# Optimization experiments

Hardware: AMD Instinct MI355X
Metric: run time of the kernel (lower is better)

The kernel has to match this reference:

```python
import jax, jax.numpy as jnp
import numpy as np

N_HEADS = 16


def setup_inputs() -> dict:
    key = jax.random.key(0)
    ks = jax.random.split(key, 8)
    ts, td, b, hc = 64, 4096, 8, 1024
    scale = 1.0 / np.sqrt(hc)
    return {
        "s": jax.random.normal(ks[0], (ts, b, hc), dtype=jnp.float32),
        "d": jax.random.normal(ks[1], (td, b, hc), dtype=jnp.float32),
        "Wq": jax.random.normal(ks[2], (hc, hc), dtype=jnp.float32) * scale,
        "bq": jax.random.normal(ks[3], (hc,), dtype=jnp.float32) * 0.01,
        "Wk": jax.random.normal(ks[4], (hc, hc), dtype=jnp.float32) * scale,
        "bk": jax.random.normal(ks[5], (hc,), dtype=jnp.float32) * 0.01,
        "Wv": jax.random.normal(ks[6], (hc, hc), dtype=jnp.float32) * scale,
        "bv": jax.random.normal(ks[7], (hc,), dtype=jnp.float32) * 0.01,
    }


def reference(s, d, Wq, bq, Wk, bk, Wv, bv):
    ts, b, hc = s.shape
    td = d.shape[0]
    h = N_HEADS
    c = hc // h
    # linear projections (torch Linear: x @ W.T + b)
    q = (s @ Wq.T + bq).reshape(ts, b, h, c)
    k = (d @ Wk.T + bk).reshape(td, b, h, c)
    v = (d @ Wv.T + bv).reshape(td, b, h, c)
    # scores over (slot, token) pairs, scaled
    a = jnp.einsum('sbhc,dbhc->sdbh', q, k) / jnp.sqrt(jnp.asarray(c, s.dtype))
    # competitive softmax across the SLOT axis (dim 0), not the key axis
    a = jax.nn.softmax(a, axis=0)          # (ts, td, b, h)
    n = jnp.sum(a, axis=1) + 0.001         # (ts, b, h)
    num = jnp.einsum('sdbh,dbhc->sbhc', a, v)
    out = num / n[..., None]               # normalized weighted average
    return out.reshape(ts, b, hc)
```

## Files before the change

### kernel.cpp

```cpp
#include <hip/hip_runtime.h>


#define TS 64
#define TD 4096
#define BATCH 8
#define HC 1024
#define NHEAD 16
#define MD (TD*BATCH)
#define MS (TS*BATCH)
#define NCHUNK 8
#define CHTOK (TD/NCHUNK)

#define KTILES 32

typedef __attribute__((ext_vector_type(8))) __bf16 bf16x8;
typedef __attribute__((ext_vector_type(4))) float f32x4;
typedef __attribute__((ext_vector_type(4))) unsigned short u16x4;
typedef __attribute__((ext_vector_type(8))) unsigned short u16x8;

__device__ __forceinline__ unsigned short f2bf(float x){
  union { float f; unsigned u; } v; v.f = x;
  unsigned r = v.u + 0x7FFFu + ((v.u >> 16) & 1u);
  return (unsigned short)(r >> 16);
}

__device__ __forceinline__ void gll16(const void* g, void* l){
  __builtin_amdgcn_global_load_lds((__attribute__((address_space(1))) void*)g,
                                   (__attribute__((address_space(3))) void*)l, 16, 0, 0);
}

__global__ void cvt_all(const float* __restrict__ d, const float* __restrict__ s,
                        const float* __restrict__ wq, const float* __restrict__ wk,
                        const float* __restrict__ wv,
                        unsigned short* __restrict__ dbf, unsigned short* __restrict__ sbf,
                        unsigned short* __restrict__ wqb, unsigned short* __restrict__ wkb,
                        unsigned short* __restrict__ wvb){
  long i = (long)blockIdx.x * 256 + threadIdx.x;
  const float* src; unsigned short* dst; long off;
  if (i < 8388608L)      { src = d;  dst = dbf; off = i; }
  else if (i < 8519680L) { src = s;  dst = sbf; off = i - 8388608L; }
  else if (i < 8781824L) { src = wq; dst = wqb; off = i - 8519680L; }
  else if (i < 9043968L) { src = wk; dst = wkb; off = i - 8781824L; }
  else                   { src = wv; dst = wvb; off = i - 9043968L; }
  f32x4 f = ((const f32x4*)src)[off];
  u16x4 o;
  o[0] = f2bf(f[0]); o[1] = f2bf(f[1]); o[2] = f2bf(f[2]); o[3] = f2bf(f[3]);
  ((u16x4*)dst)[off] = o;
}

__global__ __launch_bounds__(512, 2) void gemm_qkv(
    const unsigned short* __restrict__ A,
    const unsigned short* __restrict__ Sb,
    const unsigned short* __restrict__ Wkv,
    const unsigned short* __restrict__ Wq,
    const float* __restrict__ bq,
    const float* __restrict__ bk,
    const float* __restrict__ bv,
    unsigned short* __restrict__ Qout,
    unsigned short* __restrict__ Kout,
    unsigned short* __restrict__ Vout)
{
  __shared__ unsigned short As[4][256*32];
  __shared__ unsigned short Bs[4][256*32];

  const int nwg = gridDim.x;
  const int cpx = nwg >> 3;
  const int orig = blockIdx.x;
  const int wg = (orig & 7) * cpx + (orig >> 3);
  const int tid = threadIdx.x;
  const int lane = tid & 63, w = tid >> 6;
  const int l15 = lane & 15, lg = lane >> 4;
  const int wm = w >> 2, wn = w & 3;

  const bool isQ = (wg >= 1024);
  int mt, nt;
  const unsigned short* Ab; const unsigned short* Bb;
  if (!isQ){ mt = wg >> 3; nt = wg & 7; Ab = A;  Bb = Wkv; }
  else     { int qi = wg - 1024; mt = qi >> 2; nt = qi & 3; Ab = Sb; Bb = Wq; }

  const int lr = lane >> 2;
  const int schunk = (((lane & 3) ^ ((lane >> 3) & 3)) << 4);
  const char* pa[2]; const char* pb[2]; unsigned ldso[2];
  #pragma unroll
  for (int j = 0; j < 2; ++j){
    int grow = j*128 + w*16 + lr;
    pa[j] = (const char*)Ab + (size_t)(mt*256 + grow)*2048 + schunk;
    pb[j] = (const char*)Bb + (size_t)(nt*256 + grow)*2048 + schunk;
    ldso[j] = (unsigned)(j*8192 + w*1024);
  }

  #define STAGE_A(t) { char* dst = (char*)&As[(t)&3][0]; \
    gll16(pa[0] + (size_t)(t)*64, dst + ldso[0]); \
    gll16(pa[1] + (size_t)(t)*64, dst + ldso[1]); }
  #define STAGE_B(t) { char* dst = (char*)&Bs[(t)&3][0]; \
    gll16(pb[0] + (size_t)(t)*64, dst + ldso[0]); \
    gll16(pb[1] + (size_t)(t)*64, dst + ldso[1]); }

  const unsigned cswz = ((unsigned)(lg ^ ((l15 >> 1) & 3))) << 4;
  const unsigned aoff = (unsigned)(wm*128 + l15)*64 + cswz;
  const unsigned boff = (unsigned)(wn*64  + l15)*64 + cswz;

  const f32x4 fz = {0.f, 0.f, 0.f, 0.f};
  f32x4 acc[8][4];
  #pragma unroll
  for (int m = 0; m < 8; ++m)
    #pragma unroll
    for (int n = 0; n < 4; ++n) acc[m][n] = fz;

  STAGE_A(0) STAGE_B(0) STAGE_A(1) STAGE_B(1) STAGE_A(2) STAGE_B(2)
  asm volatile("s_waitcnt vmcnt(8)" ::: "memory");
  __builtin_amdgcn_s_barrier();
  __builtin_amdgcn_sched_barrier(0);

  #pragma unroll 1
  for (int t = 0; t < KTILES; ++t){
    const char* as = (const char*)&As[t & 3][0];
    const char* bs = (const char*)&Bs[t & 3][0];

    bf16x8 af0[4], bfr[4];
    #pragma unroll
    for (int mf = 0; mf < 4; ++mf) af0[mf] = *(const bf16x8*)(as + aoff + mf*1024u);
    #pragma unroll
    for (int nf = 0; nf < 4; ++nf) bfr[nf] = *(const bf16x8*)(bs + boff + nf*1024u);
    if (t + 3 < KTILES) STAGE_A(t + 3)
    __builtin_amdgcn_s_setprio(1);
    #pragma unroll
    for (int mf = 0; mf < 4; ++mf)
      #pragma unroll
      for (int nf = 0; nf < 4; ++nf)
        acc[mf][nf] = __builtin_amdgcn_mfma_f32_16x16x32_bf16(af0[mf], bfr[nf], acc[mf][nf], 0, 0, 0);
    __builtin_amdgcn_s_setprio(0);

    bf16x8 af1[4];
    #pragma unroll
    for (int mf = 0; mf < 4; ++mf) af1[mf] = *(const bf16x8*)(as + aoff + (4 + mf)*1024u);
    if (t + 3 < KTILES) STAGE_B(t + 3)
    __builtin_amdgcn_s_setprio(1);
    #pragma unroll
    for (int mf = 0; mf < 4; ++mf)
      #pragma unroll
      for (int nf = 0; nf < 4; ++nf)
        acc[4 + mf][nf] = __builtin_amdgcn_mfma_f32_16x16x32_bf16(af1[mf], bfr[nf], acc[4 + mf][nf], 0, 0, 0);
    __builtin_amdgcn_s_setprio(0);

    __builtin_amdgcn_sched_barrier(0);
    if (t < KTILES - 3)       { asm volatile("s_waitcnt vmcnt(8)" ::: "memory"); }
    else if (t == KTILES - 3) { asm volatile("s_waitcnt vmcnt(4)" ::: "memory"); }
    else if (t == KTILES - 2) { asm volatile("s_waitcnt vmcnt(0)" ::: "memory"); }
    __builtin_amdgcn_s_barrier();
    __builtin_amdgcn_sched_barrier(0);
  }

  int ccol; unsigned short* Cb; const float* bias;
  if (isQ)         { Cb = Qout; bias = bq; ccol = nt*256 + wn*64; }
  else if (nt < 4) { Cb = Kout; bias = bk; ccol = (nt & 3)*256 + wn*64; }
  else             { Cb = Vout; bias = bv; ccol = (nt & 3)*256 + wn*64; }
  float bvv[4];
  #pragma unroll
  for (int nf = 0; nf < 4; ++nf) bvv[nf] = bias[ccol + nf*16 + l15];
  #pragma unroll
  for (int mf = 0; mf < 8; ++mf){
    #pragma unroll
    for (int r = 0; r < 4; ++r){
      size_t row = (size_t)(mt*256 + wm*128 + mf*16 + lg*4 + r);
      unsigned short* cp = Cb + row*1024 + ccol;
      #pragma unroll
      for (int nf = 0; nf < 4; ++nf)
        cp[nf*16 + l15] = f2bf(acc[mf][nf][r] + bvv[nf]);
    }
  }
  #undef STAGE_A
  #undef STAGE_B
}

__global__ __launch_bounds__(256) void attn_kernel(
    const unsigned short* __restrict__ Q,
    const unsigned short* __restrict__ K,
    const unsigned short* __restrict__ V,
    float* __restrict__ P)
{
  __shared__ unsigned short Qs[64*64];
  __shared__ unsigned short Ks[64*64];
  __shared__ unsigned short Vt[80*64];
  __shared__ unsigned short Al[64*64];
  __shared__ float red[256];

  const int bh = blockIdx.x;
  const int chunk = blockIdx.y;
  const int bb = bh >> 4, h = bh & 15;
  const int tid = threadIdx.x;
  const int lane = tid & 63, w = tid >> 6;
  const int l15 = lane & 15, lg = lane >> 4;
  const int lrow = lane >> 3, lch = (lane & 7) << 4;

  for (int i = tid; i < 16*64; i += 256){
    int r = i >> 6;
    Vt[(64 + r)*64 + (i & 63)] = (r == 0) ? (unsigned short)0x3F80 : (unsigned short)0;
  }

  #pragma unroll
  for (int j = 0; j < 2; ++j){
    int row = w*16 + j*8 + lrow;
    int sw = lch ^ ((row & 7) << 4);
    const char* g = (const char*)Q + (size_t)(row*BATCH + bb)*2048 + h*128 + sw;
    gll16(g, (char*)Qs + (w*16 + j*8)*128);
  }

  const f32x4 fz = {0.f, 0.f, 0.f, 0.f};
  f32x4 acc[5];
  #pragma unroll
  for (int nb = 0; nb < 5; ++nb) acc[nb] = fz;

  const int vtok = tid >> 2;
  const int vcg  = tid & 3;
  const int t0 = chunk * CHTOK;

  for (int tt = 0; tt < CHTOK/64; ++tt){
    const int tb = t0 + tt*64;
    #pragma unroll
    for (int j = 0; j < 2; ++j){
      int row = w*16 + j*8 + lrow;
      int sw = lch ^ ((row & 7) << 4);
      const char* g = (const char*)K + (size_t)((size_t)(tb + row)*BATCH + bb)*2048 + h*128 + sw;
      gll16(g, (char*)Ks + (w*16 + j*8)*128);
    }
    const char* vg = (const char*)V + (size_t)((size_t)(tb + vtok)*BATCH + bb)*2048 + h*128 + vcg*32;
    u16x8 v0 = *(const u16x8*)vg;
    u16x8 v1 = *(const u16x8*)(vg + 16);
    __syncthreads();

    bf16x8 qa[2];
    #pragma unroll
    for (int kk = 0; kk < 2; ++kk){
      int row = w*16 + l15;
      qa[kk] = *(const bf16x8*)((const char*)Qs + row*128 + ((lg*16 + kk*64) ^ ((row & 7) << 4)));
    }
    float e[4][4];
    #pragma unroll
    for (int nb = 0; nb < 4; ++nb){
      f32x4 s = fz;
      #pragma unroll
      for (int kk = 0; kk < 2; ++kk){
        int row = nb*16 + l15;
        bf16x8 kb = *(const bf16x8*)((const char*)Ks + row*128 + ((lg*16 + kk*64) ^ ((row & 7) << 4)));
        s = __builtin_amdgcn_mfma_f32_16x16x32_bf16(qa[kk], kb, s, 0, 0, 0);
      }
      #pragma unroll
      for (int r = 0; r < 4; ++r) e[nb][r] = __expf(s[r] * 0.125f);
    }
    #pragma unroll
    for (int nb = 0; nb < 4; ++nb){
      float cp = e[nb][0] + e[nb][1] + e[nb][2] + e[nb][3];
      cp += __shfl_xor(cp, 16);
      cp += __shfl_xor(cp, 32);
      if (lg == 0) red[w*64 + nb*16 + l15] = cp;
    }
    __syncthreads();

    #pragma unroll
    for (int nb = 0; nb < 4; ++nb){
      int col = nb*16 + l15;
      float dn = red[col] + red[64 + col] + red[128 + col] + red[192 + col];
      float inv = 1.0f / dn;
      #pragma unroll
      for (int r = 0; r < 4; ++r){
        int row = w*16 + lg*4 + r;
        Al[row*64 + ((((2*col)) ^ ((row & 7) << 4)) >> 1)] = f2bf(e[nb][r] * inv);
      }
    }
    #pragma unroll
    for (int ee = 0; ee < 8; ++ee){
      int c0 = vcg*16 + ee;
      int sw0 = (((c0 & 7) ^ (c0 >> 3)) & 7) << 4;
      Vt[c0*64 + (((2*vtok) ^ sw0) >> 1)] = v0[ee];
    }
    #pragma unroll
    for (int ee = 0; ee < 8; ++ee){
      int c1 = vcg*16 + 8 + ee;
      int sw1 = (((c1 & 7) ^ (c1 >> 3)) & 7) << 4;
      Vt[c1*64 + (((2*vtok) ^ sw1) >> 1)] = v1[ee];
    }
    __syncthreads();

    bf16x8 aa[2];
    #pragma unroll
    for (int kk = 0; kk < 2; ++kk){
      int row = w*16 + l15;
      aa[kk] = *(const bf16x8*)((const char*)Al + row*128 + ((lg*16 + kk*64) ^ ((row & 7) << 4)));
    }
    #pragma unroll
    for (int nb = 0; nb < 5; ++nb){
      #pragma unroll
      for (int kk = 0; kk < 2; ++kk){
        int row = nb*16 + l15;
        int sw = (((row & 7) ^ (row >> 3)) & 7) << 4;
        bf16x8 vb = *(const bf16x8*)((const char*)Vt + row*128 + ((lg*16 + kk*64) ^ sw));
        acc[nb] = __builtin_amdgcn_mfma_f32_16x16x32_bf16(aa[kk], vb, acc[nb], 0, 0, 0);
      }
    }
  }

  float* Pb = P + (size_t)(bh*NCHUNK + chunk) * 64 * 80;
  #pragma unroll
  for (int nb = 0; nb < 5; ++nb){
    #pragma unroll
    for (int r = 0; r < 4; ++r){
      int s = w*16 + lg*4 + r;
      Pb[(size_t)s*80 + nb*16 + l15] = acc[nb][r];
    }
  }
}

__global__ void reduce_out(const float* __restrict__ P, float* __restrict__ out){
  int flat = blockIdx.x * 256 + threadIdx.x;
  int c = flat & 63, s = (flat >> 6) & 63, bh = flat >> 12;
  int bb = bh >> 4, h = bh & 15;
  float sc = 0.f, sn = 0.f;
  #pragma unroll
  for (int ch = 0; ch < NCHUNK; ++ch){
    const float* base = P + ((size_t)(bh*NCHUNK + ch)*64 + s)*80;
    sc += base[c];
    sn += base[64];
  }
  out[((size_t)s*BATCH + bb)*1024 + h*64 + c] = sc / (sn + 0.001f);
}

extern "C" void kernel_launch(void* const* d_in, const int* in_sizes, int n_in,
                              void* d_out, int out_size, void* d_ws, size_t ws_size,
                              hipStream_t stream)
{
  const float* s  = (const float*)d_in[0];
  const float* d  = (const float*)d_in[1];
  const float* Wq = (const float*)d_in[2];
  const float* bq = (const float*)d_in[3];
  const float* Wk = (const float*)d_in[4];
  const float* bk = (const float*)d_in[5];
  const float* Wv = (const float*)d_in[6];
  const float* bv = (const float*)d_in[7];
  float* out = (float*)d_out;

  char* ws = (char*)d_ws;
  unsigned short* dbf = (unsigned short*)(ws);
  unsigned short* sbf = (unsigned short*)(ws + 67108864);
  unsigned short* wqb = (unsigned short*)(ws + 68157440);
  unsigned short* wkb = (unsigned short*)(ws + 70254592);
  unsigned short* wvb = (unsigned short*)(ws + 72351744);
  unsigned short* Qw  = (unsigned short*)(ws + 74448896);
  unsigned short* Kw  = (unsigned short*)(ws + 75497472);
  unsigned short* Vw  = (unsigned short*)(ws + 142606336);
  float*          Pw  = (float*)(ws + 209715200);

  (void)in_sizes; (void)n_in; (void)out_size; (void)ws_size;

  cvt_all<<<36352, 256, 0, stream>>>(d, s, Wq, Wk, Wv, dbf, sbf, wqb, wkb, wvb);

  gemm_qkv<<<1032, 512, 0, stream>>>(dbf, sbf, wkb, wqb, bq, bk, bv, Qw, Kw, Vw);

  attn_kernel<<<dim3(128, NCHUNK), 256, 0, stream>>>(Qw, Kw, Vw, Pw);

  reduce_out<<<(TS*BATCH*HC)/256, 256, 0, stream>>>(Pw, out);
}
```

Before: 243.8 us.

## Fuse fp32-to-bf16 conversion of activations into QKV GEMM A-tile loading

Removes the separate conversion pass over d and s (about 128 MB read and 64 MB written). The GEMM now loads fp32 A tiles into registers one tile ahead, converts them to bf16 and writes them to LDS with the same swizzle. Only the weights still go through a small conversion kernel. In exchange, the GEMM reads twice as many A bytes, and since each d tile is read by 8 N-tile workgroups, that extra fp32 traffic depends on cache reuse. A prefetch depth shrinks from 3 stages to 1 with register staging, and each iteration adds an LDS write plus a wait.

```diff
diff --git a/kernel.cpp b/kernel.cpp
--- a/kernel.cpp
+++ b/kernel.cpp
@@ -29,19 +29,15 @@
                                    (__attribute__((address_space(3))) void*)l, 16, 0, 0);
 }
 
-__global__ void cvt_all(const float* __restrict__ d, const float* __restrict__ s,
-                        const float* __restrict__ wq, const float* __restrict__ wk,
-                        const float* __restrict__ wv,
-                        unsigned short* __restrict__ dbf, unsigned short* __restrict__ sbf,
-                        unsigned short* __restrict__ wqb, unsigned short* __restrict__ wkb,
-                        unsigned short* __restrict__ wvb){
+__global__ void cvt_w(const float* __restrict__ wq, const float* __restrict__ wk,
+                      const float* __restrict__ wv,
+                      unsigned short* __restrict__ wqb, unsigned short* __restrict__ wkb,
+                      unsigned short* __restrict__ wvb){
   long i = (long)blockIdx.x * 256 + threadIdx.x;
   const float* src; unsigned short* dst; long off;
-  if (i < 8388608L)      { src = d;  dst = dbf; off = i; }
-  else if (i < 8519680L) { src = s;  dst = sbf; off = i - 8388608L; }
-  else if (i < 8781824L) { src = wq; dst = wqb; off = i - 8519680L; }
-  else if (i < 9043968L) { src = wk; dst = wkb; off = i - 8781824L; }
-  else                   { src = wv; dst = wvb; off = i - 9043968L; }
+  if (i < 262144L)      { src = wq; dst = wqb; off = i; }
+  else if (i < 524288L) { src = wk; dst = wkb; off = i - 262144L; }
+  else                  { src = wv; dst = wvb; off = i - 524288L; }
   f32x4 f = ((const f32x4*)src)[off];
   u16x4 o;
   o[0] = f2bf(f[0]); o[1] = f2bf(f[1]); o[2] = f2bf(f[2]); o[3] = f2bf(f[3]);
@@ -49,8 +45,8 @@
 }
 
 __global__ __launch_bounds__(512, 2) void gemm_qkv(
-    const unsigned short* __restrict__ A,
-    const unsigned short* __restrict__ Sb,
+    const float* __restrict__ dA,
+    const float* __restrict__ sA,
     const unsigned short* __restrict__ Wkv,
     const unsigned short* __restrict__ Wq,
     const float* __restrict__ bq,
@@ -74,28 +70,52 @@
 
   const bool isQ = (wg >= 1024);
   int mt, nt;
-  const unsigned short* Ab; const unsigned short* Bb;
-  if (!isQ){ mt = wg >> 3; nt = wg & 7; Ab = A;  Bb = Wkv; }
-  else     { int qi = wg - 1024; mt = qi >> 2; nt = qi & 3; Ab = Sb; Bb = Wq; }
+  const float* Af; const unsigned short* Bb;
+  if (!isQ){ mt = wg >> 3; nt = wg & 7; Af = dA; Bb = Wkv; }
+  else     { int qi = wg - 1024; mt = qi >> 2; nt = qi & 3; Af = sA; Bb = Wq; }
+
+  const int lrw = lane >> 2;
+  const int c4  = lane & 3;
+  const int swp = c4 ^ ((lane >> 3) & 3);
+  const char* paf[2]; unsigned wadr[2];
+  #pragma unroll
+  for (int j = 0; j < 2; ++j){
+    int rowg = j*128 + w*16 + lrw;
+    paf[j] = (const char*)Af + (size_t)(mt*256 + rowg) * 4096 + (unsigned)(c4*32);
+    wadr[j] = (unsigned)(rowg*64 + (swp << 4));
+  }
 
   const int lr = lane >> 2;
   const int schunk = (((lane & 3) ^ ((lane >> 3) & 3)) << 4);
-  const char* pa[2]; const char* pb[2]; unsigned ldso[2];
+  const char* pb[2]; unsigned ldso[2];
   #pragma unroll
   for (int j = 0; j < 2; ++j){
     int grow = j*128 + w*16 + lr;
-    pa[j] = (const char*)Ab + (size_t)(mt*256 + grow)*2048 + schunk;
     pb[j] = (const char*)Bb + (size_t)(nt*256 + grow)*2048 + schunk;
     ldso[j] = (unsigned)(j*8192 + w*1024);
   }
 
-  #define STAGE_A(t) { char* dst = (char*)&As[(t)&3][0]; \
-    gll16(pa[0] + (size_t)(t)*64, dst + ldso[0]); \
-    gll16(pa[1] + (size_t)(t)*64, dst + ldso[1]); }
   #define STAGE_B(t) { char* dst = (char*)&Bs[(t)&3][0]; \
     gll16(pb[0] + (size_t)(t)*64, dst + ldso[0]); \
     gll16(pb[1] + (size_t)(t)*64, dst + ldso[1]); }
 
+  f32x4 la0, la1, la2, la3;
+  #define LOAD_A(tn) { \
+    la0 = *(const f32x4*)(paf[0] + (size_t)(tn)*128); \
+    la1 = *(const f32x4*)(paf[0] + (size_t)(tn)*128 + 16); \
+    la2 = *(const f32x4*)(paf[1] + (size_t)(tn)*128); \
+    la3 = *(const f32x4*)(paf[1] + (size_t)(tn)*128 + 16); }
+
+  #define CVT_WRITE_A(buf_) { \
+    char* dstA = (char*)&As[buf_][0]; \
+    bf16x8 t0, t1; \
+    t0[0]=(__bf16)la0[0]; t0[1]=(__bf16)la0[1]; t0[2]=(__bf16)la0[2]; t0[3]=(__bf16)la0[3]; \
+    t0[4]=(__bf16)la1[0]; t0[5]=(__bf16)la1[1]; t0[6]=(__bf16)la1[2]; t0[7]=(__bf16)la1[3]; \
+    t1[0]=(__bf16)la2[0]; t1[1]=(__bf16)la2[1]; t1[2]=(__bf16)la2[2]; t1[3]=(__bf16)la2[3]; \
+    t1[4]=(__bf16)la3[0]; t1[5]=(__bf16)la3[1]; t1[6]=(__bf16)la3[2]; t1[7]=(__bf16)la3[3]; \
+    *(bf16x8*)(dstA + wadr[0]) = t0; \
+    *(bf16x8*)(dstA + wadr[1]) = t1; }
+
   const unsigned cswz = ((unsigned)(lg ^ ((l15 >> 1) & 3))) << 4;
   const unsigned aoff = (unsigned)(wm*128 + l15)*64 + cswz;
   const unsigned boff = (unsigned)(wn*64  + l15)*64 + cswz;
@@ -107,8 +127,11 @@
     #pragma unroll
     for (int n = 0; n < 4; ++n) acc[m][n] = fz;
 
-  STAGE_A(0) STAGE_B(0) STAGE_A(1) STAGE_B(1) STAGE_A(2) STAGE_B(2)
-  asm volatile("s_waitcnt vmcnt(8)" ::: "memory");
+  STAGE_B(0) STAGE_B(1) STAGE_B(2)
+  LOAD_A(0)
+  CVT_WRITE_A(0)
+  asm volatile("s_waitcnt lgkmcnt(0)" ::: "memory");
+  __builtin_amdgcn_sched_barrier(0);
   __builtin_amdgcn_s_barrier();
   __builtin_amdgcn_sched_barrier(0);
 
@@ -117,12 +140,15 @@
     const char* as = (const char*)&As[t & 3][0];
     const char* bs = (const char*)&Bs[t & 3][0];
 
+    if (t + 1 < KTILES) { LOAD_A(t + 1) }
+    __builtin_amdgcn_sched_barrier(0);
+
     bf16x8 af0[4], bfr[4];
     #pragma unroll
     for (int mf = 0; mf < 4; ++mf) af0[mf] = *(const bf16x8*)(as + aoff + mf*1024u);
     #pragma unroll
     for (int nf = 0; nf < 4; ++nf) bfr[nf] = *(const bf16x8*)(bs + boff + nf*1024u);
-    if (t + 3 < KTILES) STAGE_A(t + 3)
+    if (t + 3 < KTILES) STAGE_B(t + 3)
     __builtin_amdgcn_s_setprio(1);
     #pragma unroll
     for (int mf = 0; mf < 4; ++mf)
@@ -134,7 +160,6 @@
     bf16x8 af1[4];
     #pragma unroll
     for (int mf = 0; mf < 4; ++mf) af1[mf] = *(const bf16x8*)(as + aoff + (4 + mf)*1024u);
-    if (t + 3 < KTILES) STAGE_B(t + 3)
     __builtin_amdgcn_s_setprio(1);
     #pragma unroll
     for (int mf = 0; mf < 4; ++mf)
@@ -144,8 +169,12 @@
     __builtin_amdgcn_s_setprio(0);
 
     __builtin_amdgcn_sched_barrier(0);
-    if (t < KTILES - 3)       { asm volatile("s_waitcnt vmcnt(8)" ::: "memory"); }
-    else if (t == KTILES - 3) { asm volatile("s_waitcnt vmcnt(4)" ::: "memory"); }
+    if (t + 1 < KTILES) { CVT_WRITE_A((t + 1) & 3) }
+    __builtin_amdgcn_sched_barrier(0);
+    asm volatile("s_waitcnt lgkmcnt(0)" ::: "memory");
+    __builtin_amdgcn_sched_barrier(0);
+    if (t < KTILES - 3)       { asm volatile("s_waitcnt vmcnt(4)" ::: "memory"); }
+    else if (t == KTILES - 3) { asm volatile("s_waitcnt vmcnt(2)" ::: "memory"); }
     else if (t == KTILES - 2) { asm volatile("s_waitcnt vmcnt(0)" ::: "memory"); }
     __builtin_amdgcn_s_barrier();
     __builtin_amdgcn_sched_barrier(0);
@@ -169,8 +198,9 @@
         cp[nf*16 + l15] = f2bf(acc[mf][nf][r] + bvv[nf]);
     }
   }
-  #undef STAGE_A
   #undef STAGE_B
+  #undef LOAD_A
+  #undef CVT_WRITE_A
 }
 
 __global__ __launch_bounds__(256) void attn_kernel(
@@ -340,8 +370,6 @@
   float* out = (float*)d_out;
 
   char* ws = (char*)d_ws;
-  unsigned short* dbf = (unsigned short*)(ws);
-  unsigned short* sbf = (unsigned short*)(ws + 67108864);
   unsigned short* wqb = (unsigned short*)(ws + 68157440);
   unsigned short* wkb = (unsigned short*)(ws + 70254592);
   unsigned short* wvb = (unsigned short*)(ws + 72351744);
@@ -352,9 +380,9 @@
 
   (void)in_sizes; (void)n_in; (void)out_size; (void)ws_size;
 
-  cvt_all<<<36352, 256, 0, stream>>>(d, s, Wq, Wk, Wv, dbf, sbf, wqb, wkb, wvb);
-
-  gemm_qkv<<<1032, 512, 0, stream>>>(dbf, sbf, wkb, wqb, bq, bk, bv, Qw, Kw, Vw);
+  cvt_w<<<3072, 256, 0, stream>>>(Wq, Wk, Wv, wqb, wkb, wvb);
+
+  gemm_qkv<<<1032, 512, 0, stream>>>(d, s, wkb, wqb, bq, bk, bv, Qw, Kw, Vw);
 
   attn_kernel<<<dim3(128, NCHUNK), 256, 0, stream>>>(Qw, Kw, Vw, Pw);
 
```

After: 304.8 us. 25.0% more time.

## Switch QKV GEMM to 64-wide K tiles with double buffering

Applied to the files above, without the earlier changes.

The QKV projection GEMM now stages K tiles of 64 instead of 32, with a 2-slot double buffer replacing the 4-slot ring (32KB per operand either way). The LDS swizzle is widened to 8 chunks, and the manual vmcnt waits and split A/B staging are replaced by a single combined stage and __syncthreads per iteration. This halves the number of barriers and loop iterations. In exchange the prefetch depth drops from three tiles ahead to one, and the __syncthreads waits on all outstanding loads, so global latency may be exposed.

```diff
diff --git a/kernel.cpp b/kernel.cpp
--- a/kernel.cpp
+++ b/kernel.cpp
@@ -11,7 +11,7 @@
 #define NCHUNK 8
 #define CHTOK (TD/NCHUNK)
 
-#define KTILES 32
+#define KT64 16
 
 typedef __attribute__((ext_vector_type(8))) __bf16 bf16x8;
 typedef __attribute__((ext_vector_type(4))) float f32x4;
@@ -60,8 +60,8 @@
     unsigned short* __restrict__ Kout,
     unsigned short* __restrict__ Vout)
 {
-  __shared__ unsigned short As[4][256*32];
-  __shared__ unsigned short Bs[4][256*32];
+  __shared__ unsigned short As[2][256*64];
+  __shared__ unsigned short Bs[2][256*64];
 
   const int nwg = gridDim.x;
   const int cpx = nwg >> 3;
@@ -78,27 +78,36 @@
   if (!isQ){ mt = wg >> 3; nt = wg & 7; Ab = A;  Bb = Wkv; }
   else     { int qi = wg - 1024; mt = qi >> 2; nt = qi & 3; Ab = Sb; Bb = Wq; }
 
-  const int lr = lane >> 2;
-  const int schunk = (((lane & 3) ^ ((lane >> 3) & 3)) << 4);
-  const char* pa[2]; const char* pb[2]; unsigned ldso[2];
-  #pragma unroll
-  for (int j = 0; j < 2; ++j){
-    int grow = j*128 + w*16 + lr;
+  const int ri = lane >> 3;
+  const int Sst = ((ri >> 1) & 3) | ((ri & 1) << 2);
+  const unsigned schunk = (unsigned)(((lane & 7) ^ Sst) << 4);
+  const char* pa[4]; const char* pb[4]; unsigned ldso[4];
+  #pragma unroll
+  for (int j = 0; j < 4; ++j){
+    int grow = w*32 + j*8 + ri;
     pa[j] = (const char*)Ab + (size_t)(mt*256 + grow)*2048 + schunk;
     pb[j] = (const char*)Bb + (size_t)(nt*256 + grow)*2048 + schunk;
-    ldso[j] = (unsigned)(j*8192 + w*1024);
-  }
-
-  #define STAGE_A(t) { char* dst = (char*)&As[(t)&3][0]; \
-    gll16(pa[0] + (size_t)(t)*64, dst + ldso[0]); \
-    gll16(pa[1] + (size_t)(t)*64, dst + ldso[1]); }
-  #define STAGE_B(t) { char* dst = (char*)&Bs[(t)&3][0]; \
-    gll16(pb[0] + (size_t)(t)*64, dst + ldso[0]); \
-    gll16(pb[1] + (size_t)(t)*64, dst + ldso[1]); }
-
-  const unsigned cswz = ((unsigned)(lg ^ ((l15 >> 1) & 3))) << 4;
-  const unsigned aoff = (unsigned)(wm*128 + l15)*64 + cswz;
-  const unsigned boff = (unsigned)(wn*64  + l15)*64 + cswz;
+    ldso[j] = (unsigned)((w*32 + j*8) * 128);
+  }
+
+  #define STAGE_AB(t_, sl_) { \
+    const size_t ko = (size_t)(t_) * 128; \
+    char* da = (char*)&As[sl_][0]; char* db = (char*)&Bs[sl_][0]; \
+    gll16(pa[0] + ko, da + ldso[0]); \
+    gll16(pa[1] + ko, da + ldso[1]); \
+    gll16(pa[2] + ko, da + ldso[2]); \
+    gll16(pa[3] + ko, da + ldso[3]); \
+    gll16(pb[0] + ko, db + ldso[0]); \
+    gll16(pb[1] + ko, db + ldso[1]); \
+    gll16(pb[2] + ko, db + ldso[2]); \
+    gll16(pb[3] + ko, db + ldso[3]); \
+    __builtin_amdgcn_sched_barrier(0); }
+
+  const int Sr = ((l15 >> 1) & 3) | ((l15 & 1) << 2);
+  const unsigned ck0 = (unsigned)(((0 + lg) ^ Sr) << 4);
+  const unsigned ck1 = (unsigned)(((4 + lg) ^ Sr) << 4);
+  const unsigned arow = (unsigned)(wm*128 + l15) * 128;
+  const unsigned brow = (unsigned)(wn*64  + l15) * 128;
 
   const f32x4 fz = {0.f, 0.f, 0.f, 0.f};
   f32x4 acc[8][4];
@@ -107,48 +116,41 @@
     #pragma unroll
     for (int n = 0; n < 4; ++n) acc[m][n] = fz;
 
-  STAGE_A(0) STAGE_B(0) STAGE_A(1) STAGE_B(1) STAGE_A(2) STAGE_B(2)
-  asm volatile("s_waitcnt vmcnt(8)" ::: "memory");
-  __builtin_amdgcn_s_barrier();
-  __builtin_amdgcn_sched_barrier(0);
+  #define HALF(as_, bs_, ckh_) { \
+    bf16x8 af0[4], bfr[4]; \
+    _Pragma("unroll") \
+    for (int mf = 0; mf < 4; ++mf) af0[mf] = *(const bf16x8*)(as_ + arow + mf*2048u + (ckh_)); \
+    _Pragma("unroll") \
+    for (int nf = 0; nf < 4; ++nf) bfr[nf] = *(const bf16x8*)(bs_ + brow + nf*2048u + (ckh_)); \
+    __builtin_amdgcn_s_setprio(1); \
+    _Pragma("unroll") \
+    for (int mf = 0; mf < 4; ++mf) \
+      _Pragma("unroll") \
+      for (int nf = 0; nf < 4; ++nf) \
+        acc[mf][nf] = __builtin_amdgcn_mfma_f32_16x16x32_bf16(af0[mf], bfr[nf], acc[mf][nf], 0, 0, 0); \
+    __builtin_amdgcn_s_setprio(0); \
+    bf16x8 af1[4]; \
+    _Pragma("unroll") \
+    for (int mf = 0; mf < 4; ++mf) af1[mf] = *(const bf16x8*)(as_ + arow + (4 + mf)*2048u + (ckh_)); \
+    __builtin_amdgcn_s_setprio(1); \
+    _Pragma("unroll") \
+    for (int mf = 0; mf < 4; ++mf) \
+      _Pragma("unroll") \
+      for (int nf = 0; nf < 4; ++nf) \
+        acc[4 + mf][nf] = __builtin_amdgcn_mfma_f32_16x16x32_bf16(af1[mf], bfr[nf], acc[4 + mf][nf], 0, 0, 0); \
+    __builtin_amdgcn_s_setprio(0); }
+
+  STAGE_AB(0, 0)
+  __syncthreads();
 
   #pragma unroll 1
-  for (int t = 0; t < KTILES; ++t){
-    const char* as = (const char*)&As[t & 3][0];
-    const char* bs = (const char*)&Bs[t & 3][0];
-
-    bf16x8 af0[4], bfr[4];
-    #pragma unroll
-    for (int mf = 0; mf < 4; ++mf) af0[mf] = *(const bf16x8*)(as + aoff + mf*1024u);
-    #pragma unroll
-    for (int nf = 0; nf < 4; ++nf) bfr[nf] = *(const bf16x8*)(bs + boff + nf*1024u);
-    if (t + 3 < KTILES) STAGE_A(t + 3)
-    __builtin_amdgcn_s_setprio(1);
-    #pragma unroll
-    for (int mf = 0; mf < 4; ++mf)
-      #pragma unroll
-      for (int nf = 0; nf < 4; ++nf)
-        acc[mf][nf] = __builtin_amdgcn_mfma_f32_16x16x32_bf16(af0[mf], bfr[nf], acc[mf][nf], 0, 0, 0);
-    __builtin_amdgcn_s_setprio(0);
-
-    bf16x8 af1[4];
-    #pragma unroll
-    for (int mf = 0; mf < 4; ++mf) af1[mf] = *(const bf16x8*)(as + aoff + (4 + mf)*1024u);
-    if (t + 3 < KTILES) STAGE_B(t + 3)
-    __builtin_amdgcn_s_setprio(1);
-    #pragma unroll
-    for (int mf = 0; mf < 4; ++mf)
-      #pragma unroll
-      for (int nf = 0; nf < 4; ++nf)
-        acc[4 + mf][nf] = __builtin_amdgcn_mfma_f32_16x16x32_bf16(af1[mf], bfr[nf], acc[4 + mf][nf], 0, 0, 0);
-    __builtin_amdgcn_s_setprio(0);
-
-    __builtin_amdgcn_sched_barrier(0);
-    if (t < KTILES - 3)       { asm volatile("s_waitcnt vmcnt(8)" ::: "memory"); }
-    else if (t == KTILES - 3) { asm volatile("s_waitcnt vmcnt(4)" ::: "memory"); }
-    else if (t == KTILES - 2) { asm volatile("s_waitcnt vmcnt(0)" ::: "memory"); }
-    __builtin_amdgcn_s_barrier();
-    __builtin_amdgcn_sched_barrier(0);
+  for (int t = 0; t < KT64; ++t){
+    if (t + 1 < KT64) STAGE_AB(t + 1, (t + 1) & 1)
+    const char* as = (const char*)&As[t & 1][0];
+    const char* bs = (const char*)&Bs[t & 1][0];
+    HALF(as, bs, ck0)
+    HALF(as, bs, ck1)
+    __syncthreads();
   }
 
   int ccol; unsigned short* Cb; const float* bias;
@@ -169,8 +171,8 @@
         cp[nf*16 + l15] = f2bf(acc[mf][nf][r] + bvv[nf]);
     }
   }
-  #undef STAGE_A
-  #undef STAGE_B
+  #undef STAGE_AB
+  #undef HALF
 }
 
 __global__ __launch_bounds__(256) void attn_kernel(
```

Result: slower. 260.9 us (+7.0%).
